# Performance work log

Measured on AMD Instinct MI355X. Metric: run time of the kernel, lower is better.

## Reference

```python
import jax, jax.numpy as jnp
import numpy as np


def setup_inputs() -> dict:
    key = jax.random.key(0)
    k1, k2, k3 = jax.random.split(key, 3)
    B, T, D = 4, 8192, 1024
    x = jax.random.normal(k1, (B, T, D), dtype=jnp.float32)
    decay = jax.random.normal(k2, (D,), dtype=jnp.float32)
    freq = jax.random.normal(k3, (D,), dtype=jnp.float32)
    return {"x": x, "decay": decay, "freq": freq}


def reference(x, decay, freq):
    B, T, D = x.shape
    t = jnp.arange(T, dtype=jnp.float32)  # [T]
    # learned decaying-cosine kernel, shape [T, D]
    k = jnp.exp(-jnp.abs(decay)[None, :] * t[:, None]) * jnp.cos(freq[None, :] * t[:, None])
    n_fft = 2 * T  # zero-pad to 2T for linear (causal) convolution
    x_f = jnp.fft.rfft(x, n=n_fft, axis=1)          # [B, T+1, D] complex
    k_f = jnp.fft.rfft(k, n=n_fft, axis=0)          # [T+1, D] complex
    y = jnp.fft.irfft(x_f * k_f[None, :, :], n=n_fft, axis=1)
    return y[:, :T, :]
```

## Files before the change

kernel.cpp:

```cpp
#include <hip/hip_runtime.h>
#include <math.h>


#define D_DIM 1024

typedef float floatx4 __attribute__((ext_vector_type(4)));

struct RPow {
  float cr1[4], ci1[4];
  float cr2[4], ci2[4];
  float cr3[4], ci3[4];
  float cr4[4], ci4[4];
};

__device__ __forceinline__ void load_rpow(const float* __restrict__ decay,
                                          const float* __restrict__ freq, int d,
                                          RPow& P) {
  float4 dv = *(const float4*)(decay + d);
  float4 fv = *(const float4*)(freq + d);
  float a[4] = {dv.x, dv.y, dv.z, dv.w};
  float w[4] = {fv.x, fv.y, fv.z, fv.w};
#pragma unroll
  for (int k = 0; k < 4; ++k) {
    float ak = fabsf(a[k]);
    float e = expf(-ak);
    float rr = e * cosf(w[k]);
    float ri = e * sinf(w[k]);
    P.cr1[k] = rr;
    P.ci1[k] = ri;
    float r2r = fmaf(rr, rr, -ri * ri);
    float r2i = 2.f * rr * ri;
    P.cr2[k] = r2r;
    P.ci2[k] = r2i;
    P.cr3[k] = fmaf(r2r, rr, -r2i * ri);
    P.ci3[k] = fmaf(r2r, ri, r2i * rr);
    P.cr4[k] = fmaf(r2r, r2r, -r2i * r2i);
    P.ci4[k] = 2.f * r2r * r2i;
  }
}

__global__ __launch_bounds__(256, 4) void carry_kernel(
    const float* __restrict__ x, const float* __restrict__ decay,
    const float* __restrict__ freq, float2* __restrict__ zloc,
    int T, int L, int C) {
  const int c = blockIdx.x;
  const int b = blockIdx.y;
  const int d = threadIdx.x * 4;

  RPow P;
  load_rpow(decay, freq, d, P);

  const float4* xp =
      (const float4*)(x + ((size_t)b * T + (size_t)c * L) * D_DIM + d);
  const size_t stride = D_DIM / 4;

  float zr[4] = {0.f, 0.f, 0.f, 0.f}, zi[4] = {0.f, 0.f, 0.f, 0.f};
  const int G = L >> 2;
#pragma unroll 2
  for (int g = 0; g < G; ++g) {
    const float4* xg = xp + (size_t)g * 4 * stride;
    float4 v0 = xg[0];
    float4 v1 = xg[stride];
    float4 v2 = xg[2 * stride];
    float4 v3 = xg[3 * stride];
    float X0[4] = {v0.x, v0.y, v0.z, v0.w};
    float X1[4] = {v1.x, v1.y, v1.z, v1.w};
    float X2[4] = {v2.x, v2.y, v2.z, v2.w};
    float X3[4] = {v3.x, v3.y, v3.z, v3.w};
#pragma unroll
    for (int k = 0; k < 4; ++k) {
      float sr = fmaf(P.cr3[k], X0[k], fmaf(P.cr2[k], X1[k], fmaf(P.cr1[k], X2[k], X3[k])));
      float si = fmaf(P.ci3[k], X0[k], fmaf(P.ci2[k], X1[k], P.ci1[k] * X2[k]));
      float nr = fmaf(P.cr4[k], zr[k], fmaf(-P.ci4[k], zi[k], sr));
      float ni = fmaf(P.cr4[k], zi[k], fmaf(P.ci4[k], zr[k], si));
      zr[k] = nr;
      zi[k] = ni;
    }
  }

  float4* zp = (float4*)(zloc + ((size_t)b * C + c) * D_DIM + d);
  zp[0] = make_float4(zr[0], zi[0], zr[1], zi[1]);
  zp[1] = make_float4(zr[2], zi[2], zr[3], zi[3]);
}

__global__ __launch_bounds__(256) void scan_kernel(
    const float* __restrict__ decay, const float* __restrict__ freq,
    float2* __restrict__ zloc, int L, int C) {
  const int b = blockIdx.y;
  const int dbase = blockIdx.x * 32;
  const int tid = threadIdx.x;

  __shared__ float2 A[32][257];
  __shared__ float2 RLP[8][32];

  {
    int k = tid >> 5, d = tid & 31;
    float a = fabsf(decay[dbase + d]);
    float w = freq[dbase + d];
    float m = (float)L * (float)(1 << k);
    float e = expf(-a * m);
    RLP[k][d] = make_float2(e * cosf(w * m), e * sinf(w * m));
  }

  {
    int d = tid & 31;
    for (int j = tid >> 5; j < C; j += 8) {
      A[d][j] = zloc[((size_t)b * C + j) * D_DIM + dbase + d];
    }
  }
  __syncthreads();

  const int c = tid;
  const bool own = (c < C);
  float2 I[32];
  if (own) {
#pragma unroll
    for (int d = 0; d < 32; ++d) I[d] = A[d][c];
  }

  for (int k = 0; (1 << k) < C; ++k) {
    const int off = 1 << k;
    if (own && c >= off) {
#pragma unroll
      for (int d = 0; d < 32; ++d) {
        float2 p = A[d][c - off];
        float2 m = RLP[k][d];
        I[d].x = fmaf(m.x, p.x, fmaf(-m.y, p.y, I[d].x));
        I[d].y = fmaf(m.x, p.y, fmaf(m.y, p.x, I[d].y));
      }
    }
    __syncthreads();
    if (own) {
#pragma unroll
      for (int d = 0; d < 32; ++d) A[d][c] = I[d];
    }
    __syncthreads();
  }

  {
    int d = tid & 31;
    for (int j = tid >> 5; j < C; j += 8) {
      float2 v = (j == 0) ? make_float2(0.f, 0.f) : A[d][j - 1];
      zloc[((size_t)b * C + j) * D_DIM + dbase + d] = v;
    }
  }
}

__global__ __launch_bounds__(256, 4) void final_kernel(
    const float* __restrict__ x, const float* __restrict__ decay,
    const float* __restrict__ freq, const float2* __restrict__ zloc,
    float* __restrict__ y, int T, int L, int C) {
  const int c = blockIdx.x;
  const int b = blockIdx.y;
  const int d = threadIdx.x * 4;

  RPow P;
  load_rpow(decay, freq, d, P);

  const float2* zl = zloc + ((size_t)b * C + c) * D_DIM + d;
  float4 z0 = *(const float4*)(zl);
  float4 z1 = *(const float4*)(zl + 2);
  float zr[4] = {z0.x, z0.z, z1.x, z1.z};
  float zi[4] = {z0.y, z0.w, z1.y, z1.w};

  const size_t off = ((size_t)b * T + (size_t)c * L) * D_DIM + d;
  const float4* xp = (const float4*)(x + off);
  floatx4* yp = (floatx4*)(y + off);
  const size_t stride = D_DIM / 4;

  const int G = L >> 2;
#pragma unroll 2
  for (int g = 0; g < G; ++g) {
    const float4* xg = xp + (size_t)g * 4 * stride;
    float4 v0 = xg[0];
    float4 v1 = xg[stride];
    float4 v2 = xg[2 * stride];
    float4 v3 = xg[3 * stride];
    float X0[4] = {v0.x, v0.y, v0.z, v0.w};
    float X1[4] = {v1.x, v1.y, v1.z, v1.w};
    float X2[4] = {v2.x, v2.y, v2.z, v2.w};
    float X3[4] = {v3.x, v3.y, v3.z, v3.w};
    float Y0[4], Y1[4], Y2[4], Y3[4];
#pragma unroll
    for (int k = 0; k < 4; ++k) {
      Y0[k] = fmaf(P.cr1[k], zr[k], fmaf(-P.ci1[k], zi[k], X0[k]));
      Y1[k] = fmaf(P.cr2[k], zr[k],
                   fmaf(-P.ci2[k], zi[k], fmaf(P.cr1[k], X0[k], X1[k])));
      Y2[k] = fmaf(P.cr3[k], zr[k],
                   fmaf(-P.ci3[k], zi[k],
                        fmaf(P.cr2[k], X0[k], fmaf(P.cr1[k], X1[k], X2[k]))));
      float sr = fmaf(P.cr3[k], X0[k], fmaf(P.cr2[k], X1[k], fmaf(P.cr1[k], X2[k], X3[k])));
      float si = fmaf(P.ci3[k], X0[k], fmaf(P.ci2[k], X1[k], P.ci1[k] * X2[k]));
      float nr = fmaf(P.cr4[k], zr[k], fmaf(-P.ci4[k], zi[k], sr));
      float ni = fmaf(P.cr4[k], zi[k], fmaf(P.ci4[k], zr[k], si));
      zr[k] = nr;
      zi[k] = ni;
      Y3[k] = nr;
    }
    floatx4 o0 = {Y0[0], Y0[1], Y0[2], Y0[3]};
    floatx4 o1 = {Y1[0], Y1[1], Y1[2], Y1[3]};
    floatx4 o2 = {Y2[0], Y2[1], Y2[2], Y2[3]};
    floatx4 o3 = {Y3[0], Y3[1], Y3[2], Y3[3]};
    floatx4* yg = yp + (size_t)g * 4 * stride;
    __builtin_nontemporal_store(o0, &yg[0]);
    __builtin_nontemporal_store(o1, &yg[stride]);
    __builtin_nontemporal_store(o2, &yg[2 * stride]);
    __builtin_nontemporal_store(o3, &yg[3 * stride]);
  }
}

extern "C" void kernel_launch(void* const* d_in, const int* in_sizes, int n_in,
                              void* d_out, int out_size, void* d_ws, size_t ws_size,
                              hipStream_t stream) {
  const float* x     = (const float*)d_in[0];
  const float* decay = (const float*)d_in[1];
  const float* freq  = (const float*)d_in[2];
  float* y = (float*)d_out;

  const int B = 4, T = 8192;

  int C = 256;
  while (C > 1 && (size_t)B * C * D_DIM * sizeof(float2) > ws_size) C >>= 1;
  int L = T / C;

  float2* zloc = (float2*)d_ws;

  if (C > 1) {
    dim3 gc(C - 1, B);
    carry_kernel<<<gc, 256, 0, stream>>>(x, decay, freq, zloc, T, L, C);
  }
  scan_kernel<<<dim3(D_DIM / 32, B), 256, 0, stream>>>(decay, freq, zloc, L, C);
  final_kernel<<<dim3(C, B), 256, 0, stream>>>(x, decay, freq, zloc, y, T, L, C);
}
```

Baseline: 287.4 us.

## Fuse carry, scan, and output passes into one cooperative kernel with grid syncs

```diff
diff --git a/kernel.cpp b/kernel.cpp
--- a/kernel.cpp
+++ b/kernel.cpp
@@ -1,10 +1,20 @@
 #include <hip/hip_runtime.h>
+#include <hip/hip_cooperative_groups.h>
 #include <math.h>
 
+namespace cg = cooperative_groups;
+
 
 #define D_DIM 1024
+#define T_LEN 8192
+#define B_BATCH 4
+#define C_CHUNKS 128
+#define L_CHUNK (T_LEN / C_CHUNKS)
+#define G_GROUPS (L_CHUNK / 4)
 
 typedef float floatx4 __attribute__((ext_vector_type(4)));
+
+#define XSTRIDE ((size_t)(D_DIM / 4))
 
 struct RPow {
   float cr1[4], ci1[4];
@@ -39,174 +49,260 @@
   }
 }
 
-__global__ __launch_bounds__(256, 4) void carry_kernel(
+__device__ __forceinline__ void pub2(float2* p, float xr, float xi) {
+  unsigned long long u = (unsigned long long)__float_as_uint(xr) |
+                         ((unsigned long long)__float_as_uint(xi) << 32);
+  __hip_atomic_store((unsigned long long*)p, u, __ATOMIC_RELAXED,
+                     __HIP_MEMORY_SCOPE_AGENT);
+}
+__device__ __forceinline__ float2 rd2(const float2* p) {
+  unsigned long long u = __hip_atomic_load(
+      (unsigned long long*)p, __ATOMIC_RELAXED, __HIP_MEMORY_SCOPE_AGENT);
+  return make_float2(__uint_as_float((unsigned)(u & 0xffffffffull)),
+                     __uint_as_float((unsigned)(u >> 32)));
+}
+
+#define LOADG(xq, gi, R0, R1, R2, R3)                    \
+  {                                                      \
+    const float4* _p = (xq) + (size_t)(gi) * 4 * XSTRIDE;\
+    R0 = _p[0];                                          \
+    R1 = _p[XSTRIDE];                                    \
+    R2 = _p[2 * XSTRIDE];                                \
+    R3 = _p[3 * XSTRIDE];                                \
+  }
+
+#define STOREG(yp, gi, O0, O1, O2, O3)                   \
+  {                                                      \
+    floatx4* _q = (yp) + (size_t)(gi) * 4 * XSTRIDE;     \
+    __builtin_nontemporal_store(O0, _q);                 \
+    __builtin_nontemporal_store(O1, _q + XSTRIDE);       \
+    __builtin_nontemporal_store(O2, _q + 2 * XSTRIDE);   \
+    __builtin_nontemporal_store(O3, _q + 3 * XSTRIDE);   \
+  }
+
+__device__ __forceinline__ void step_carry(const RPow& P, const float4& v0,
+                                           const float4& v1, const float4& v2,
+                                           const float4& v3, float zr[4],
+                                           float zi[4]) {
+  const float X0[4] = {v0.x, v0.y, v0.z, v0.w};
+  const float X1[4] = {v1.x, v1.y, v1.z, v1.w};
+  const float X2[4] = {v2.x, v2.y, v2.z, v2.w};
+  const float X3[4] = {v3.x, v3.y, v3.z, v3.w};
+#pragma unroll
+  for (int k = 0; k < 4; ++k) {
+    float sr = fmaf(P.cr3[k], X0[k],
+                    fmaf(P.cr2[k], X1[k], fmaf(P.cr1[k], X2[k], X3[k])));
+    float si = fmaf(P.ci3[k], X0[k], fmaf(P.ci2[k], X1[k], P.ci1[k] * X2[k]));
+    float nr = fmaf(P.cr4[k], zr[k], fmaf(-P.ci4[k], zi[k], sr));
+    float ni = fmaf(P.cr4[k], zi[k], fmaf(P.ci4[k], zr[k], si));
+    zr[k] = nr;
+    zi[k] = ni;
+  }
+}
+
+__device__ __forceinline__ void step_out(const RPow& P, const float4& v0,
+                                         const float4& v1, const float4& v2,
+                                         const float4& v3, float zr[4],
+                                         float zi[4], floatx4& o0, floatx4& o1,
+                                         floatx4& o2, floatx4& o3) {
+  const float X0[4] = {v0.x, v0.y, v0.z, v0.w};
+  const float X1[4] = {v1.x, v1.y, v1.z, v1.w};
+  const float X2[4] = {v2.x, v2.y, v2.z, v2.w};
+  const float X3[4] = {v3.x, v3.y, v3.z, v3.w};
+#pragma unroll
+  for (int k = 0; k < 4; ++k) {
+    float y0 = fmaf(P.cr1[k], zr[k], fmaf(-P.ci1[k], zi[k], X0[k]));
+    float y1 = fmaf(P.cr2[k], zr[k],
+                    fmaf(-P.ci2[k], zi[k], fmaf(P.cr1[k], X0[k], X1[k])));
+    float y2 = fmaf(P.cr3[k], zr[k],
+                    fmaf(-P.ci3[k], zi[k],
+                         fmaf(P.cr2[k], X0[k], fmaf(P.cr1[k], X1[k], X2[k]))));
+    float sr = fmaf(P.cr3[k], X0[k],
+                    fmaf(P.cr2[k], X1[k], fmaf(P.cr1[k], X2[k], X3[k])));
+    float si = fmaf(P.ci3[k], X0[k], fmaf(P.ci2[k], X1[k], P.ci1[k] * X2[k]));
+    float nr = fmaf(P.cr4[k], zr[k], fmaf(-P.ci4[k], zi[k], sr));
+    float ni = fmaf(P.cr4[k], zi[k], fmaf(P.ci4[k], zr[k], si));
+    zr[k] = nr;
+    zi[k] = ni;
+    o0[k] = y0;
+    o1[k] = y1;
+    o2[k] = y2;
+    o3[k] = nr;
+  }
+}
+
+__device__ __forceinline__ void phaseA(const float* __restrict__ x,
+                                       float2* __restrict__ agg, const RPow& P,
+                                       int c, int b, int d) {
+  const size_t xoff = ((size_t)b * T_LEN + (size_t)c * L_CHUNK) * D_DIM + d;
+  const float4* xq = (const float4*)(x + xoff);
+
+  float zr[4] = {0.f, 0.f, 0.f, 0.f}, zi[4] = {0.f, 0.f, 0.f, 0.f};
+  float4 A0, A1, A2, A3, B0, B1, B2, B3;
+  LOADG(xq, 0, A0, A1, A2, A3);
+  LOADG(xq, 1, B0, B1, B2, B3);
+#pragma unroll
+  for (int g = 0; g < G_GROUPS; g += 2) {
+    step_carry(P, A0, A1, A2, A3, zr, zi);
+    if (g + 2 < G_GROUPS) LOADG(xq, g + 2, A0, A1, A2, A3);
+    step_carry(P, B0, B1, B2, B3, zr, zi);
+    if (g + 3 < G_GROUPS) LOADG(xq, g + 3, B0, B1, B2, B3);
+  }
+
+  float2* ap = agg + ((size_t)(b * C_CHUNKS + c)) * D_DIM + d;
+  pub2(ap + 0, zr[0], zi[0]);
+  pub2(ap + 1, zr[1], zi[1]);
+  pub2(ap + 2, zr[2], zi[2]);
+  pub2(ap + 3, zr[3], zi[3]);
+}
+
+__device__ __forceinline__ void phaseB(const float* __restrict__ decay,
+                                       const float* __restrict__ freq,
+                                       float2* __restrict__ agg, int slab,
+                                       int b, int tid) {
+  __shared__ float2 A[8][C_CHUNKS + 2];
+  const int dbase = slab * 8;
+
+  {
+    int dd = tid & 7;
+    for (int j = tid >> 3; j < C_CHUNKS; j += 32)
+      A[dd][j] = rd2(agg + ((size_t)(b * C_CHUNKS + j)) * D_DIM + dbase + dd);
+  }
+
+  float Mr[8], Mi[8];
+#pragma unroll
+  for (int q = 0; q < 8; ++q) {
+    float aq = fabsf(decay[dbase + q]);
+    float wq = freq[dbase + q];
+    float e = expf(-aq * (float)L_CHUNK);
+    Mr[q] = e * cosf(wq * (float)L_CHUNK);
+    Mi[q] = e * sinf(wq * (float)L_CHUNK);
+  }
+  __syncthreads();
+
+  const int cc = tid;
+  const bool own = (cc < C_CHUNKS);
+  float Ir[8], Ii[8];
+  if (own) {
+#pragma unroll
+    for (int q = 0; q < 8; ++q) {
+      float2 v = A[q][cc];
+      Ir[q] = v.x;
+      Ii[q] = v.y;
+    }
+  }
+
+#pragma unroll
+  for (int k = 0; k < 7; ++k) {
+    const int off = 1 << k;
+    if (own && cc >= off) {
+#pragma unroll
+      for (int q = 0; q < 8; ++q) {
+        float2 p = A[q][cc - off];
+        Ir[q] = fmaf(Mr[q], p.x, fmaf(-Mi[q], p.y, Ir[q]));
+        Ii[q] = fmaf(Mr[q], p.y, fmaf(Mi[q], p.x, Ii[q]));
+      }
+    }
+    __syncthreads();
+    if (own) {
+#pragma unroll
+      for (int q = 0; q < 8; ++q) A[q][cc] = make_float2(Ir[q], Ii[q]);
+    }
+    __syncthreads();
+#pragma unroll
+    for (int q = 0; q < 8; ++q) {
+      float nr = fmaf(Mr[q], Mr[q], -Mi[q] * Mi[q]);
+      Mi[q] = 2.f * Mr[q] * Mi[q];
+      Mr[q] = nr;
+    }
+  }
+
+  {
+    int dd = tid & 7;
+    for (int j = tid >> 3; j < C_CHUNKS; j += 32) {
+      float pr = 0.f, pi = 0.f;
+      if (j > 0) {
+        float2 v = A[dd][j - 1];
+        pr = v.x;
+        pi = v.y;
+      }
+      pub2(agg + ((size_t)(b * C_CHUNKS + j)) * D_DIM + dbase + dd, pr, pi);
+    }
+  }
+}
+
+__device__ __forceinline__ void phaseC(const float* __restrict__ x,
+                                       float* __restrict__ y,
+                                       const float2* __restrict__ agg,
+                                       const RPow& P, int c, int b, int d) {
+  const size_t xoff = ((size_t)b * T_LEN + (size_t)c * L_CHUNK) * D_DIM + d;
+  const float4* xq = (const float4*)(x + xoff);
+  floatx4* yp = (floatx4*)(y + xoff);
+
+  const float2* ap = agg + ((size_t)(b * C_CHUNKS + c)) * D_DIM + d;
+  float2 q0 = rd2(ap + 0), q1 = rd2(ap + 1), q2 = rd2(ap + 2), q3 = rd2(ap + 3);
+  float zr[4] = {q0.x, q1.x, q2.x, q3.x};
+  float zi[4] = {q0.y, q1.y, q2.y, q3.y};
+
+  float4 A0, A1, A2, A3, B0, B1, B2, B3;
+  LOADG(xq, 0, A0, A1, A2, A3);
+  LOADG(xq, 1, B0, B1, B2, B3);
+#pragma unroll
+  for (int g = 0; g < G_GROUPS; g += 2) {
+    floatx4 o0, o1, o2, o3;
+    step_out(P, A0, A1, A2, A3, zr, zi, o0, o1, o2, o3);
+    if (g + 2 < G_GROUPS) LOADG(xq, g + 2, A0, A1, A2, A3);
+    STOREG(yp, g, o0, o1, o2, o3);
+    floatx4 p0, p1, p2, p3;
+    step_out(P, B0, B1, B2, B3, zr, zi, p0, p1, p2, p3);
+    if (g + 3 < G_GROUPS) LOADG(xq, g + 3, B0, B1, B2, B3);
+    STOREG(yp, g + 1, p0, p1, p2, p3);
+  }
+}
+
+__global__ __launch_bounds__(256, 2) void fused_kernel(
     const float* __restrict__ x, const float* __restrict__ decay,
-    const float* __restrict__ freq, float2* __restrict__ zloc,
-    int T, int L, int C) {
-  const int c = blockIdx.x;
-  const int b = blockIdx.y;
-  const int d = threadIdx.x * 4;
+    const float* __restrict__ freq, float2* __restrict__ agg,
+    float* __restrict__ y) {
+  cg::grid_group grid = cg::this_grid();
+  const int c = blockIdx.x, b = blockIdx.y, tid = threadIdx.x;
+  const int d = tid * 4;
 
   RPow P;
   load_rpow(decay, freq, d, P);
 
-  const float4* xp =
-      (const float4*)(x + ((size_t)b * T + (size_t)c * L) * D_DIM + d);
-  const size_t stride = D_DIM / 4;
-
-  float zr[4] = {0.f, 0.f, 0.f, 0.f}, zi[4] = {0.f, 0.f, 0.f, 0.f};
-  const int G = L >> 2;
-#pragma unroll 2
-  for (int g = 0; g < G; ++g) {
-    const float4* xg = xp + (size_t)g * 4 * stride;
-    float4 v0 = xg[0];
-    float4 v1 = xg[stride];
-    float4 v2 = xg[2 * stride];
-    float4 v3 = xg[3 * stride];
-    float X0[4] = {v0.x, v0.y, v0.z, v0.w};
-    float X1[4] = {v1.x, v1.y, v1.z, v1.w};
-    float X2[4] = {v2.x, v2.y, v2.z, v2.w};
-    float X3[4] = {v3.x, v3.y, v3.z, v3.w};
-#pragma unroll
-    for (int k = 0; k < 4; ++k) {
-      float sr = fmaf(P.cr3[k], X0[k], fmaf(P.cr2[k], X1[k], fmaf(P.cr1[k], X2[k], X3[k])));
-      float si = fmaf(P.ci3[k], X0[k], fmaf(P.ci2[k], X1[k], P.ci1[k] * X2[k]));
-      float nr = fmaf(P.cr4[k], zr[k], fmaf(-P.ci4[k], zi[k], sr));
-      float ni = fmaf(P.cr4[k], zi[k], fmaf(P.ci4[k], zr[k], si));
-      zr[k] = nr;
-      zi[k] = ni;
-    }
-  }
-
-  float4* zp = (float4*)(zloc + ((size_t)b * C + c) * D_DIM + d);
-  zp[0] = make_float4(zr[0], zi[0], zr[1], zi[1]);
-  zp[1] = make_float4(zr[2], zi[2], zr[3], zi[3]);
-}
-
-__global__ __launch_bounds__(256) void scan_kernel(
-    const float* __restrict__ decay, const float* __restrict__ freq,
-    float2* __restrict__ zloc, int L, int C) {
-  const int b = blockIdx.y;
-  const int dbase = blockIdx.x * 32;
-  const int tid = threadIdx.x;
-
-  __shared__ float2 A[32][257];
-  __shared__ float2 RLP[8][32];
-
-  {
-    int k = tid >> 5, d = tid & 31;
-    float a = fabsf(decay[dbase + d]);
-    float w = freq[dbase + d];
-    float m = (float)L * (float)(1 << k);
-    float e = expf(-a * m);
-    RLP[k][d] = make_float2(e * cosf(w * m), e * sinf(w * m));
-  }
-
-  {
-    int d = tid & 31;
-    for (int j = tid >> 5; j < C; j += 8) {
-      A[d][j] = zloc[((size_t)b * C + j) * D_DIM + dbase + d];
-    }
-  }
-  __syncthreads();
-
-  const int c = tid;
-  const bool own = (c < C);
-  float2 I[32];
-  if (own) {
-#pragma unroll
-    for (int d = 0; d < 32; ++d) I[d] = A[d][c];
-  }
-
-  for (int k = 0; (1 << k) < C; ++k) {
-    const int off = 1 << k;
-    if (own && c >= off) {
-#pragma unroll
-      for (int d = 0; d < 32; ++d) {
-        float2 p = A[d][c - off];
-        float2 m = RLP[k][d];
-        I[d].x = fmaf(m.x, p.x, fmaf(-m.y, p.y, I[d].x));
-        I[d].y = fmaf(m.x, p.y, fmaf(m.y, p.x, I[d].y));
-      }
-    }
-    __syncthreads();
-    if (own) {
-#pragma unroll
-      for (int d = 0; d < 32; ++d) A[d][c] = I[d];
-    }
-    __syncthreads();
-  }
-
-  {
-    int d = tid & 31;
-    for (int j = tid >> 5; j < C; j += 8) {
-      float2 v = (j == 0) ? make_float2(0.f, 0.f) : A[d][j - 1];
-      zloc[((size_t)b * C + j) * D_DIM + dbase + d] = v;
-    }
-  }
-}
-
-__global__ __launch_bounds__(256, 4) void final_kernel(
+  phaseA(x, agg, P, c, b, d);
+  grid.sync();
+  phaseB(decay, freq, agg, c, b, tid);
+  grid.sync();
+  phaseC(x, y, agg, P, c, b, d);
+}
+
+__global__ __launch_bounds__(256, 2) void k_carry(
     const float* __restrict__ x, const float* __restrict__ decay,
-    const float* __restrict__ freq, const float2* __restrict__ zloc,
-    float* __restrict__ y, int T, int L, int C) {
-  const int c = blockIdx.x;
-  const int b = blockIdx.y;
-  const int d = threadIdx.x * 4;
-
+    const float* __restrict__ freq, float2* __restrict__ agg) {
+  const int c = blockIdx.x, b = blockIdx.y, tid = threadIdx.x;
+  const int d = tid * 4;
   RPow P;
   load_rpow(decay, freq, d, P);
-
-  const float2* zl = zloc + ((size_t)b * C + c) * D_DIM + d;
-  float4 z0 = *(const float4*)(zl);
-  float4 z1 = *(const float4*)(zl + 2);
-  float zr[4] = {z0.x, z0.z, z1.x, z1.z};
-  float zi[4] = {z0.y, z0.w, z1.y, z1.w};
-
-  const size_t off = ((size_t)b * T + (size_t)c * L) * D_DIM + d;
-  const float4* xp = (const float4*)(x + off);
-  floatx4* yp = (floatx4*)(y + off);
-  const size_t stride = D_DIM / 4;
-
-  const int G = L >> 2;
-#pragma unroll 2
-  for (int g = 0; g < G; ++g) {
-    const float4* xg = xp + (size_t)g * 4 * stride;
-    float4 v0 = xg[0];
-    float4 v1 = xg[stride];
-    float4 v2 = xg[2 * stride];
-    float4 v3 = xg[3 * stride];
-    float X0[4] = {v0.x, v0.y, v0.z, v0.w};
-    float X1[4] = {v1.x, v1.y, v1.z, v1.w};
-    float X2[4] = {v2.x, v2.y, v2.z, v2.w};
-    float X3[4] = {v3.x, v3.y, v3.z, v3.w};
-    float Y0[4], Y1[4], Y2[4], Y3[4];
-#pragma unroll
-    for (int k = 0; k < 4; ++k) {
-      Y0[k] = fmaf(P.cr1[k], zr[k], fmaf(-P.ci1[k], zi[k], X0[k]));
-      Y1[k] = fmaf(P.cr2[k], zr[k],
-                   fmaf(-P.ci2[k], zi[k], fmaf(P.cr1[k], X0[k], X1[k])));
-      Y2[k] = fmaf(P.cr3[k], zr[k],
-                   fmaf(-P.ci3[k], zi[k],
-                        fmaf(P.cr2[k], X0[k], fmaf(P.cr1[k], X1[k], X2[k]))));
-      float sr = fmaf(P.cr3[k], X0[k], fmaf(P.cr2[k], X1[k], fmaf(P.cr1[k], X2[k], X3[k])));
-      float si = fmaf(P.ci3[k], X0[k], fmaf(P.ci2[k], X1[k], P.ci1[k] * X2[k]));
-      float nr = fmaf(P.cr4[k], zr[k], fmaf(-P.ci4[k], zi[k], sr));
-      float ni = fmaf(P.cr4[k], zi[k], fmaf(P.ci4[k], zr[k], si));
-      zr[k] = nr;
-      zi[k] = ni;
-      Y3[k] = nr;
-    }
-    floatx4 o0 = {Y0[0], Y0[1], Y0[2], Y0[3]};
-    floatx4 o1 = {Y1[0], Y1[1], Y1[2], Y1[3]};
-    floatx4 o2 = {Y2[0], Y2[1], Y2[2], Y2[3]};
-    floatx4 o3 = {Y3[0], Y3[1], Y3[2], Y3[3]};
-    floatx4* yg = yp + (size_t)g * 4 * stride;
-    __builtin_nontemporal_store(o0, &yg[0]);
-    __builtin_nontemporal_store(o1, &yg[stride]);
-    __builtin_nontemporal_store(o2, &yg[2 * stride]);
-    __builtin_nontemporal_store(o3, &yg[3 * stride]);
-  }
+  phaseA(x, agg, P, c, b, d);
+}
+
+__global__ __launch_bounds__(256) void k_scan(
+    const float* __restrict__ decay, const float* __restrict__ freq,
+    float2* __restrict__ agg) {
+  phaseB(decay, freq, agg, blockIdx.x, blockIdx.y, threadIdx.x);
+}
+
+__global__ __launch_bounds__(256, 2) void k_final(
+    const float* __restrict__ x, const float* __restrict__ decay,
+    const float* __restrict__ freq, const float2* __restrict__ agg,
+    float* __restrict__ y) {
+  const int c = blockIdx.x, b = blockIdx.y, tid = threadIdx.x;
+  const int d = tid * 4;
+  RPow P;
+  load_rpow(decay, freq, d, P);
+  phaseC(x, y, agg, P, c, b, d);
 }
 
 extern "C" void kernel_launch(void* const* d_in, const int* in_sizes, int n_in,
@@ -217,18 +313,16 @@
   const float* freq  = (const float*)d_in[2];
   float* y = (float*)d_out;
 
-  const int B = 4, T = 8192;
-
-  int C = 256;
-  while (C > 1 && (size_t)B * C * D_DIM * sizeof(float2) > ws_size) C >>= 1;
-  int L = T / C;
-
-  float2* zloc = (float2*)d_ws;
-
-  if (C > 1) {
-    dim3 gc(C - 1, B);
-    carry_kernel<<<gc, 256, 0, stream>>>(x, decay, freq, zloc, T, L, C);
-  }
-  scan_kernel<<<dim3(D_DIM / 32, B), 256, 0, stream>>>(decay, freq, zloc, L, C);
-  final_kernel<<<dim3(C, B), 256, 0, stream>>>(x, decay, freq, zloc, y, T, L, C);
-}
+  float2* agg = (float2*)d_ws;
+
+  dim3 grid(C_CHUNKS, B_BATCH), block(256);
+  void* args[] = {(void*)&x, (void*)&decay, (void*)&freq, (void*)&agg,
+                  (void*)&y};
+  hipError_t err = hipLaunchCooperativeKernel((const void*)fused_kernel, grid,
+                                              block, args, 0, stream);
+  if (err != hipSuccess) {
+    k_carry<<<grid, block, 0, stream>>>(x, decay, freq, agg);
+    k_scan<<<grid, block, 0, stream>>>(decay, freq, agg);
+    k_final<<<grid, block, 0, stream>>>(x, decay, freq, agg, y);
+  }
+}
```

Result: slower. 391.7 us (+36.3%).
